# Performance work log

Measured on AMD Instinct MI355X. Metric: run time of the kernel, lower is better.

The kernel has to match this reference:

```python
import jax, jax.numpy as jnp
import numpy as np

EPS = 1e-6
B, P, C, H = 2, 2048, 256, 8
HD = C // H            # head_dims = 32
CH = C * 4             # mlp hidden = 1024


def _ln(x, g, b):
    mu = x.mean(-1, keepdims=True)
    var = ((x - mu) ** 2).mean(-1, keepdims=True)
    return (x - mu) / jnp.sqrt(var + EPS) * g + b


def _bn(x, g, b):
    # BatchNorm1d training mode on (B, Ch, L) == normalize (B,L) per channel of (B,L,Ch)
    mu = x.mean((0, 1))
    var = ((x - mu) ** 2).mean((0, 1))
    return (x - mu) / jnp.sqrt(var + EPS) * g + b


def setup_inputs() -> dict:
    key = jax.random.key(0)
    ks = jax.random.split(key, 16)
    s = 0.02
    d = {
        'x': jax.random.normal(ks[0], (B, P, C), jnp.float32),
        'ln1_g': jnp.ones((C,), jnp.float32), 'ln1_b': jnp.zeros((C,), jnp.float32),
        'ln2_g': jnp.ones((C,), jnp.float32), 'ln2_b': jnp.zeros((C,), jnp.float32),
        'Wq': jax.random.normal(ks[1], (C, C), jnp.float32) * s,
        'bq': jnp.zeros((C,), jnp.float32),
        'Wk': jax.random.normal(ks[2], (C, C), jnp.float32) * s,
        'bk': jnp.zeros((C,), jnp.float32),
        'Wv': jax.random.normal(ks[3], (C, C), jnp.float32) * s,
        'bv': jnp.zeros((C,), jnp.float32),
        'Wp': jax.random.normal(ks[4], (C, C), jnp.float32) * s,
        'bp': jnp.zeros((C,), jnp.float32),
        'W1': jax.random.normal(ks[5], (C, CH), jnp.float32) * s,
        'b1': jnp.zeros((CH,), jnp.float32),
        'bn1_g': jnp.ones((CH,), jnp.float32), 'bn1_b': jnp.zeros((CH,), jnp.float32),
        'W2': jax.random.normal(ks[6], (CH, C), jnp.float32) * s,
        'b2': jnp.zeros((C,), jnp.float32),
        'bn2_g': jnp.ones((C,), jnp.float32), 'bn2_b': jnp.zeros((C,), jnp.float32),
    }
    return d


def reference(x, ln1_g, ln1_b, ln2_g, ln2_b, Wq, bq, Wk, bk, Wv, bv, Wp, bp,
              W1, b1, bn1_g, bn1_b, W2, b2, bn2_g, bn2_b):
    lnx = _ln(x, ln1_g, ln1_b)
    # NOTE: channel-interleaved head split (view(B,P,HD,H)), faithful to source
    q = (lnx @ Wq + bq).reshape(B, P, HD, H)
    k = (lnx @ Wk + bk).reshape(B, P, HD, H)
    v = (lnx @ Wv + bv).reshape(B, P, HD, H)
    scores = jnp.einsum('bqdh,bkdh->bhqk', q, k) / np.sqrt(HD).astype(np.float32)
    w = jax.nn.softmax(scores, axis=-1)                       # (B,H,P,P)
    head = jnp.einsum('bhqk,bkdh->bhqd', w, v)                # (B,H,P,HD)
    # torch.cat(heads, -1): head0 block first -> (B,P,H,HD) flatten
    attn = head.transpose(0, 2, 1, 3).reshape(B, P, C) @ Wp + bp
    x = x + attn
    ln2x = _ln(x, ln2_g, ln2_b)
    h = jax.nn.gelu(_bn(ln2x @ W1 + b1, bn1_g, bn1_b), approximate=False)
    h = _bn(h @ W2 + b2, bn2_g, bn2_b)
    x = x + h
    fuse_weights = w[:, H - 1]          # last head's softmax weights (B,P,P)
    fuse_v = v[:, :, :, H - 1]          # last head's values (B,P,HD)
    return (x, fuse_weights, fuse_v)
```

## Files before the change

### kernel.cpp

```cpp
#include <hip/hip_runtime.h>
#include <math.h>

typedef __attribute__((ext_vector_type(8))) __bf16 bf16x8;
typedef __attribute__((ext_vector_type(4))) float f32x4;

#define NROWS 4096
#define NCe   1048576

__global__ __launch_bounds__(256) void prep_kernel(
    const float* __restrict__ Wq, const float* __restrict__ Wk,
    const float* __restrict__ Wv, const float* __restrict__ Wp,
    const float* __restrict__ W1, const float* __restrict__ W2,
    const float* __restrict__ bq, const float* __restrict__ bk,
    const float* __restrict__ bv,
    __bf16* __restrict__ wqkvT, __bf16* __restrict__ wpT,
    __bf16* __restrict__ w1T, __bf16* __restrict__ w2T,
    float* __restrict__ bqkv)
{
    int bid = blockIdx.x;
    if (bid == 768) {
        for (int i=0;i<3;i++){
            int t = i*256 + threadIdx.x;
            int h = (t>>5)&7, d = t&31;
            int c = d*8 + h;
            const float* bsrc = (t<256) ? bq : (t<512 ? bk : bv);
            bqkv[t] = bsrc[c];
        }
        return;
    }
    const float* src; __bf16* dst; int R, C, tr, tc;
    bool permute = false;
    if (bid < 256) {
        int which = bid>>6, t = bid&63;
        src = (which==0)?Wq:(which==1)?Wk:(which==2)?Wv:Wp;
        dst = (which<3) ? (wqkvT + which*65536) : wpT;
        permute = (which<3);
        R=256; C=256; tr=t>>3; tc=t&7;
    } else if (bid < 512) {
        int t = bid-256; src=W1; dst=w1T; R=256; C=1024; tr=t>>5; tc=t&31;
    } else {
        int t = bid-512; src=W2; dst=w2T; R=1024; C=256; tr=t>>3; tc=t&7;
    }
    __shared__ float tile[32][33];
    int r = threadIdx.x>>5, c = threadIdx.x&31;
    #pragma unroll
    for (int i=0;i<4;i++)
        tile[r + i*8][c] = src[(size_t)(tr*32 + r + i*8)*C + tc*32 + c];
    __syncthreads();
    #pragma unroll
    for (int i=0;i<4;i++){
        int n = tc*32 + i*8 + r;
        int nn = permute ? (((n&7)<<5) | (n>>3)) : n;
        dst[(size_t)nn*R + tr*32 + c] = (__bf16)tile[c][i*8 + r];
    }
}

__global__ __launch_bounds__(256) void ln_kernel(const float* __restrict__ x,
        const float* __restrict__ g, const float* __restrict__ b,
        __bf16* __restrict__ out)
{
    int row = blockIdx.x, t = threadIdx.x;
    float v = x[(size_t)row*256 + t];
    __shared__ float red[4];
    float s = v;
    #pragma unroll
    for (int off=32; off; off>>=1) s += __shfl_xor(s, off, 64);
    int wave = t>>6, lane = t&63;
    if (lane==0) red[wave]=s;
    __syncthreads();
    float mu = (red[0]+red[1]+red[2]+red[3]) * (1.f/256);
    float d = v - mu;
    float s2 = d*d;
    #pragma unroll
    for (int off=32; off; off>>=1) s2 += __shfl_xor(s2, off, 64);
    __syncthreads();
    if (lane==0) red[wave]=s2;
    __syncthreads();
    float var = (red[0]+red[1]+red[2]+red[3]) * (1.f/256);
    out[(size_t)row*256 + t] = (__bf16)(d * rsqrtf(var + 1e-6f) * g[t] + b[t]);
}

template<int EP>
__global__ __launch_bounds__(256) void mm_kernel(
    const __bf16* __restrict__ A, const __bf16* __restrict__ Bt,
    const float* __restrict__ bias, const float* __restrict__ resid,
    void* __restrict__ outp, float* __restrict__ out2,
    int M, int N, int K)
{
    __shared__ __bf16 Alds[128*64];
    __shared__ __bf16 Blds[128*64];
    const int tid = threadIdx.x;
    const int bm = blockIdx.y*128, bn = blockIdx.x*128;
    const int w = tid>>6, l = tid&63;
    const int wr = w>>1, wc = w&1;
    const int lg = l>>4, ll = l&15;
    f32x4 acc[4][4] = {};
    int sr[4], sc[4];
    #pragma unroll
    for (int i=0;i<4;i++){ int s = tid + i*256; sr[i]=s>>3; sc[i]=s&7; }

    for (int k0=0; k0<K; k0+=64){
        bf16x8 av[4], bv[4];
        #pragma unroll
        for (int i=0;i<4;i++){
            av[i] = *(const bf16x8*)(A  + (size_t)(bm+sr[i])*K + k0 + sc[i]*8);
            bv[i] = *(const bf16x8*)(Bt + (size_t)(bn+sr[i])*K + k0 + sc[i]*8);
        }
        __syncthreads();
        #pragma unroll
        for (int i=0;i<4;i++){
            int cc = sc[i] ^ (sr[i]&7);
            *(bf16x8*)(&Alds[sr[i]*64 + cc*8]) = av[i];
            *(bf16x8*)(&Blds[sr[i]*64 + cc*8]) = bv[i];
        }
        __syncthreads();
        #pragma unroll
        for (int kk=0; kk<2; kk++){
            bf16x8 af[4], bfr[4];
            #pragma unroll
            for (int t=0;t<4;t++){
                int ar = wr*64 + t*16 + ll;
                int ac = (kk*4 + lg) ^ (ar&7);
                af[t] = *(const bf16x8*)(&Alds[ar*64 + ac*8]);
                int br = wc*64 + t*16 + ll;
                int bc = (kk*4 + lg) ^ (br&7);
                bfr[t] = *(const bf16x8*)(&Blds[br*64 + bc*8]);
            }
            #pragma unroll
            for (int i=0;i<4;i++)
                #pragma unroll
                for (int j=0;j<4;j++)
                    acc[i][j] = __builtin_amdgcn_mfma_f32_16x16x32_bf16(af[i], bfr[j], acc[i][j], 0,0,0);
        }
    }
    #pragma unroll
    for (int i=0;i<4;i++){
        #pragma unroll
        for (int j=0;j<4;j++){
            #pragma unroll
            for (int r=0;r<4;r++){
                int m = bm + wr*64 + i*16 + lg*4 + r;
                int n = bn + wc*64 + j*16 + ll;
                float val = acc[i][j][r] + bias[n];
                if (EP == 0){
                    int kind = n>>8, h = (n>>5)&7, d = n&31;
                    int b = m>>11, p = m&2047;
                    __bf16* q = (__bf16*)outp;
                    size_t addr = (((size_t)(b*8+h))*2048 + p)*32 + d;
                    if (kind==0)      q[addr] = (__bf16)val;
                    else if (kind==1) q[NCe + addr] = (__bf16)val;
                    else {
                        q[2*NCe + addr] = (__bf16)val;
                        if (h==7) out2[((size_t)(b*2048+p))*32 + d] = val;
                    }
                } else {
                    ((__bf16*)outp)[(size_t)m*N + n] = (__bf16)val;
                }
            }
        }
    }
}

template<int EP>
__global__ __launch_bounds__(256) void mm64_kernel(
    const __bf16* __restrict__ A, const __bf16* __restrict__ Bt,
    const float* __restrict__ bias, const float* __restrict__ resid,
    void* __restrict__ outp, int M, int N, int K)
{
    __shared__ __bf16 Alds[64*64];
    __shared__ __bf16 Blds[64*64];
    const int tid = threadIdx.x;
    const int bm = blockIdx.y*64, bn = blockIdx.x*64;
    const int w = tid>>6, l = tid&63;
    const int lg = l>>4, ll = l&15;
    f32x4 acc[4] = {};
    int sr[2], sc[2];
    #pragma unroll
    for (int i=0;i<2;i++){ int s = tid + i*256; sr[i]=s>>3; sc[i]=s&7; }

    for (int k0=0; k0<K; k0+=64){
        bf16x8 av[2], bv[2];
        #pragma unroll
        for (int i=0;i<2;i++){
            av[i] = *(const bf16x8*)(A  + (size_t)(bm+sr[i])*K + k0 + sc[i]*8);
            bv[i] = *(const bf16x8*)(Bt + (size_t)(bn+sr[i])*K + k0 + sc[i]*8);
        }
        __syncthreads();
        #pragma unroll
        for (int i=0;i<2;i++){
            int cc = sc[i] ^ (sr[i]&7);
            *(bf16x8*)(&Alds[sr[i]*64 + cc*8]) = av[i];
            *(bf16x8*)(&Blds[sr[i]*64 + cc*8]) = bv[i];
        }
        __syncthreads();
        #pragma unroll
        for (int kk=0; kk<2; kk++){
            int ar = w*16 + ll;
            int ac = (kk*4 + lg) ^ (ar&7);
            bf16x8 af = *(const bf16x8*)(&Alds[ar*64 + ac*8]);
            #pragma unroll
            for (int j=0;j<4;j++){
                int br = j*16 + ll;
                int bc = (kk*4 + lg) ^ (br&7);
                bf16x8 bfr = *(const bf16x8*)(&Blds[br*64 + bc*8]);
                acc[j] = __builtin_amdgcn_mfma_f32_16x16x32_bf16(af, bfr, acc[j], 0,0,0);
            }
        }
        __syncthreads();
    }
    #pragma unroll
    for (int j=0;j<4;j++){
        #pragma unroll
        for (int r=0;r<4;r++){
            int m = bm + w*16 + lg*4 + r;
            int n = bn + j*16 + ll;
            float val = acc[j][r] + bias[n];
            if (EP == 1){
                size_t idx = (size_t)m*N + n;
                ((float*)outp)[idx] = val + resid[idx];
            } else {
                ((__bf16*)outp)[(size_t)m*N + n] = (__bf16)val;
            }
        }
    }
}

__global__ __launch_bounds__(256) void vtrans_kernel(
    const __bf16* __restrict__ vh, __bf16* __restrict__ vt)
{
    int bh = blockIdx.x>>5, d = blockIdx.x&31;
    const __bf16* src = vh + (size_t)bh*65536 + d;
    __bf16* dst = vt + (size_t)bh*65536 + (size_t)d*2048;
    int tid = threadIdx.x;
    bf16x8 v;
    #pragma unroll
    for (int j=0;j<8;j++) v[j] = src[(size_t)(tid*8+j)*32];
    *(bf16x8*)(dst + tid*8) = v;
}

__global__ __launch_bounds__(256) void attn_kernel(
    const __bf16* __restrict__ qh, const __bf16* __restrict__ kh,
    const __bf16* __restrict__ vt, __bf16* __restrict__ Oc,
    float* __restrict__ lbuf)
{
    __shared__ __bf16 Klds[64*32];
    __shared__ __bf16 Vlds[32*64];
    __shared__ __bf16 Plds[4][16*72];
    const float kScale = 0.17677669529663687f;
    int tid = threadIdx.x, w = tid>>6, l = tid&63;
    int lg = l>>4, ll = l&15;
    int bh = blockIdx.y;
    int q0 = blockIdx.x*64 + w*16;
    const __bf16* Qh = qh + (size_t)bh*65536;
    const __bf16* Kh = kh + (size_t)bh*65536;
    const __bf16* Vh = vt + (size_t)bh*65536;
    bf16x8 qf = *(const bf16x8*)(Qh + (size_t)(q0 + ll)*32 + lg*8);
    f32x4 o0 = {0,0,0,0}, o1 = {0,0,0,0};
    float lrow[4] = {0,0,0,0};
    int kr = tid>>2, kc = tid&3;
    int vr = tid>>3, vc = tid&7;
    __bf16* P = Plds[w];
    for (int kt=0; kt<2048; kt+=64){
        bf16x8 kv = *(const bf16x8*)(Kh + (size_t)(kt + kr)*32 + kc*8);
        bf16x8 vv = *(const bf16x8*)(Vh + (size_t)vr*2048 + kt + vc*8);
        __syncthreads();
        *(bf16x8*)(&Klds[kr*32 + (kc ^ ((kr>>1)&3))*8]) = kv;
        *(bf16x8*)(&Vlds[vr*64 + (vc ^ (vr&7))*8]) = vv;
        __syncthreads();
        f32x4 s[4];
        #pragma unroll
        for (int t=0;t<4;t++){
            int krow = t*16 + ll;
            bf16x8 kf = *(const bf16x8*)(&Klds[krow*32 + (lg ^ ((krow>>1)&3))*8]);
            f32x4 z = {0,0,0,0};
            s[t] = __builtin_amdgcn_mfma_f32_16x16x32_bf16(qf, kf, z, 0,0,0);
        }
        #pragma unroll
        for (int t=0;t<4;t++){
            #pragma unroll
            for (int r=0;r<4;r++){
                float p = __expf(s[t][r]*kScale);
                lrow[r] += p;
                P[(lg*4+r)*72 + t*16 + ll] = (__bf16)p;
            }
        }
        #pragma unroll
        for (int kc2=0;kc2<2;kc2++){
            bf16x8 pf = *(const bf16x8*)(&P[ll*72 + kc2*32 + lg*8]);
            int vch = kc2*4 + lg;
            int vrow0 = ll;
            bf16x8 vf0 = *(const bf16x8*)(&Vlds[vrow0*64 + (vch ^ (vrow0&7))*8]);
            o0 = __builtin_amdgcn_mfma_f32_16x16x32_bf16(pf, vf0, o0, 0,0,0);
            int vrow1 = 16 + ll;
            bf16x8 vf1 = *(const bf16x8*)(&Vlds[vrow1*64 + (vch ^ (vrow1&7))*8]);
            o1 = __builtin_amdgcn_mfma_f32_16x16x32_bf16(pf, vf1, o1, 0,0,0);
        }
    }
    #pragma unroll
    for (int r=0;r<4;r++){
        float sum = lrow[r];
        sum += __shfl_xor(sum,1,64);
        sum += __shfl_xor(sum,2,64);
        sum += __shfl_xor(sum,4,64);
        sum += __shfl_xor(sum,8,64);
        lrow[r] = sum;
    }
    int b = bh>>3, h = bh&7;
    #pragma unroll
    for (int r=0;r<4;r++){
        float inv = 1.f/lrow[r];
        int p = q0 + lg*4 + r;
        size_t base = ((size_t)(b*2048 + p))*256 + h*32;
        Oc[base + ll]      = (__bf16)(o0[r]*inv);
        Oc[base + 16 + ll] = (__bf16)(o1[r]*inv);
        if (ll==0) lbuf[(size_t)bh*2048 + p] = lrow[r];
    }
}

__global__ __launch_bounds__(256) void w7_kernel(const __bf16* __restrict__ qh,
    const __bf16* __restrict__ kh, const float* __restrict__ lbuf,
    float* __restrict__ out1)
{
    __shared__ float Qs[16][32];
    __shared__ float Li[16];
    __shared__ float Ks[256][33];
    int tid = threadIdx.x;
    int b = blockIdx.x>>7, q0 = (blockIdx.x&127)*16;
    int bh = b*8+7;
    const __bf16* Kb = kh + (size_t)bh*65536;
    const float kScale = 0.17677669529663687f;
    #pragma unroll
    for (int i=0;i<2;i++){
        int e = i*256 + tid;
        Qs[e>>5][e&31] = (float)qh[((size_t)bh*2048 + q0 + (e>>5))*32 + (e&31)];
    }
    if (tid<16) Li[tid] = 1.f/lbuf[(size_t)bh*2048 + q0 + tid];

    for (int kt=0; kt<2048; kt+=256){
        __syncthreads();
        #pragma unroll
        for (int i=0;i<4;i++){
            int e = i*256 + tid;
            int row = e>>2, d0 = (e&3)*8;
            bf16x8 kv = *(const bf16x8*)(Kb + (size_t)(kt+row)*32 + d0);
            #pragma unroll
            for (int j=0;j<8;j++) Ks[row][d0+j] = (float)kv[j];
        }
        __syncthreads();
        #pragma unroll 4
        for (int ql=0; ql<16; ql++){
            float a = 0.f;
            #pragma unroll
            for (int d=0; d<32; d++) a = fmaf(Qs[ql][d], Ks[tid][d], a);
            out1[((size_t)(b*2048 + q0 + ql))*2048 + kt + tid] =
                __expf(a*kScale)*Li[ql];
        }
    }
}

template<int NCH, int RPB>
__global__ __launch_bounds__(256) void bn_stats(const __bf16* __restrict__ h,
                                                float* __restrict__ sums)
{
    int c  = blockIdx.x*256 + threadIdx.x;
    int r0 = blockIdx.y*RPB;
    float s = 0.f, s2 = 0.f;
    #pragma unroll
    for (int i=0;i<RPB;i++){
        float v = (float)h[(size_t)(r0+i)*NCH + c];
        s += v; s2 = fmaf(v,v,s2);
    }
    atomicAdd(&sums[c], s);
    atomicAdd(&sums[NCH+c], s2);
}

template<bool GELU, bool RESID, bool OUTF32>
__global__ __launch_bounds__(256) void bn_apply(const __bf16* __restrict__ hin,
    const float* __restrict__ sums, const float* __restrict__ g,
    const float* __restrict__ bb, const float* __restrict__ resid,
    void* __restrict__ outp, int Nch)
{
    size_t i0 = ((size_t)blockIdx.x*256 + threadIdx.x)*8;
    int c0 = (int)(i0 & (size_t)(Nch-1));
    bf16x8 v = *(const bf16x8*)(hin + i0);
    float res[8];
    #pragma unroll
    for (int j=0;j<8;j++){
        int c = c0+j;
        float mu  = sums[c]*(1.f/NROWS);
        float var = sums[Nch+c]*(1.f/NROWS) - mu*mu;
        float f = ((float)v[j]-mu)*rsqrtf(var+1e-6f)*g[c]+bb[c];
        if (GELU) f = 0.5f*f*(1.f+erff(f*0.70710678118654752f));
        res[j] = f;
    }
    if (RESID){
        f32x4 r0 = *(const f32x4*)(resid+i0);
        f32x4 r1 = *(const f32x4*)(resid+i0+4);
        res[0]+=r0[0]; res[1]+=r0[1]; res[2]+=r0[2]; res[3]+=r0[3];
        res[4]+=r1[0]; res[5]+=r1[1]; res[6]+=r1[2]; res[7]+=r1[3];
    }
    if (OUTF32){
        f32x4 a = {res[0],res[1],res[2],res[3]};
        f32x4 b2 = {res[4],res[5],res[6],res[7]};
        *(f32x4*)((float*)outp + i0) = a;
        *(f32x4*)((float*)outp + i0 + 4) = b2;
    } else {
        bf16x8 ov;
        #pragma unroll
        for (int j=0;j<8;j++) ov[j] = (__bf16)res[j];
        *(bf16x8*)((__bf16*)outp + i0) = ov;
    }
}

extern "C" void kernel_launch(void* const* d_in, const int* in_sizes, int n_in,
                              void* d_out, int out_size, void* d_ws, size_t ws_size,
                              hipStream_t stream) {
    (void)in_sizes; (void)n_in; (void)out_size; (void)ws_size;
    const float* x    = (const float*)d_in[0];
    const float* ln1g = (const float*)d_in[1];
    const float* ln1b = (const float*)d_in[2];
    const float* ln2g = (const float*)d_in[3];
    const float* ln2b = (const float*)d_in[4];
    const float* Wq = (const float*)d_in[5];
    const float* bq = (const float*)d_in[6];
    const float* Wk = (const float*)d_in[7];
    const float* bk = (const float*)d_in[8];
    const float* Wv = (const float*)d_in[9];
    const float* bv = (const float*)d_in[10];
    const float* Wp = (const float*)d_in[11];
    const float* bp = (const float*)d_in[12];
    const float* W1 = (const float*)d_in[13];
    const float* b1 = (const float*)d_in[14];
    const float* bn1g = (const float*)d_in[15];
    const float* bn1b = (const float*)d_in[16];
    const float* W2 = (const float*)d_in[17];
    const float* b2 = (const float*)d_in[18];
    const float* bn2g = (const float*)d_in[19];
    const float* bn2b = (const float*)d_in[20];

    float* out0 = (float*)d_out;
    float* out1 = out0 + (size_t)NROWS*256;
    float* out2 = out1 + (size_t)2*2048*2048;

    __bf16* lnx = (__bf16*)d_ws;
    __bf16* qh  = lnx + NCe;
    __bf16* kh  = qh  + NCe;
    __bf16* vt  = kh  + NCe;
    __bf16* Oc  = vt  + NCe;
    __bf16* h1  = Oc  + NCe;
    __bf16* h1g = h1  + (size_t)NROWS*1024;
    __bf16* h2  = h1g + (size_t)NROWS*1024;
    float*  x2  = (float*)(h2 + NCe);
    float*  mbuf = x2 + NCe;
    float*  lbuf = mbuf + 32768;
    float*  bns  = lbuf + 32768;
    float*  bns2 = bns + 2048;
    float*  bqkv = bns2 + 512;
    __bf16* wqkvT = (__bf16*)(bqkv + 768);
    __bf16* wpT = wqkvT + 196608;
    __bf16* w1T = wpT + 65536;
    __bf16* w2T = w1T + 262144;
    __bf16* vh  = w2T + 262144;

    dim3 blk(256);

    hipLaunchKernelGGL(prep_kernel, dim3(769), blk, 0, stream,
        Wq,Wk,Wv,Wp,W1,W2,bq,bk,bv, wqkvT,wpT,w1T,w2T,bqkv);
    hipLaunchKernelGGL(ln_kernel, dim3(NROWS), blk, 0, stream, x, ln1g, ln1b, lnx);
    hipLaunchKernelGGL((mm_kernel<0>), dim3(6,32), blk, 0, stream,
        lnx, wqkvT, bqkv, nullptr, (void*)qh, out2, NROWS, 768, 256);
    hipLaunchKernelGGL(vtrans_kernel, dim3(512), blk, 0, stream, vh, vt);
    hipLaunchKernelGGL(attn_kernel, dim3(32,16), blk, 0, stream, qh, kh, vt, Oc, lbuf);
    hipLaunchKernelGGL(w7_kernel, dim3(256), blk, 0, stream, qh, kh, lbuf, out1);
    hipLaunchKernelGGL((mm64_kernel<1>), dim3(4,64), blk, 0, stream,
        Oc, wpT, bp, x, (void*)x2, NROWS, 256, 256);
    hipLaunchKernelGGL(ln_kernel, dim3(NROWS), blk, 0, stream, x2, ln2g, ln2b, lnx);
    hipLaunchKernelGGL((mm_kernel<2>), dim3(8,32), blk, 0, stream,
        lnx, w1T, b1, nullptr, (void*)h1, nullptr, NROWS, 1024, 256);
    hipMemsetAsync(bns, 0, 2048*sizeof(float), stream);
    hipLaunchKernelGGL((bn_stats<1024,16>), dim3(4,256), blk, 0, stream, h1, bns);
    hipLaunchKernelGGL((bn_apply<true,false,false>), dim3(2048), blk, 0, stream,
        h1, bns, bn1g, bn1b, nullptr, (void*)h1g, 1024);
    hipLaunchKernelGGL((mm64_kernel<2>), dim3(4,64), blk, 0, stream,
        h1g, w2T, b2, nullptr, (void*)h2, NROWS, 256, 1024);
    hipMemsetAsync(bns2, 0, 512*sizeof(float), stream);
    hipLaunchKernelGGL((bn_stats<256,16>), dim3(1,256), blk, 0, stream, h2, bns2);
    hipLaunchKernelGGL((bn_apply<false,true,true>), dim3(512), blk, 0, stream,
        h2, bns2, bn2g, bn2b, x2, (void*)out0, 256);
}
```

Measured before the change: 288.4 us.

## Prefetch next K tile into registers in GEMM and attention loops; merge memsets

The GEMM kernels and the attention kernel now issue the global loads for the next tile into registers right after the LDS store barrier, so those loads overlap the MFMA compute on the current tile. In mm64 the trailing barrier is removed, since the barrier before the LDS store already orders reuse. The two BN-stat memsets are merged into one issued early. The cost is higher register pressure, which could lower occupancy.

Result: faster. 279.6 us (-3.1%).

```diff
diff --git a/kernel.cpp b/kernel.cpp
--- a/kernel.cpp
+++ b/kernel.cpp
@@ -99,13 +99,13 @@
     #pragma unroll
     for (int i=0;i<4;i++){ int s = tid + i*256; sr[i]=s>>3; sc[i]=s&7; }
 
+    bf16x8 av[4], bv[4];
+    #pragma unroll
+    for (int i=0;i<4;i++){
+        av[i] = *(const bf16x8*)(A  + (size_t)(bm+sr[i])*K + sc[i]*8);
+        bv[i] = *(const bf16x8*)(Bt + (size_t)(bn+sr[i])*K + sc[i]*8);
+    }
     for (int k0=0; k0<K; k0+=64){
-        bf16x8 av[4], bv[4];
-        #pragma unroll
-        for (int i=0;i<4;i++){
-            av[i] = *(const bf16x8*)(A  + (size_t)(bm+sr[i])*K + k0 + sc[i]*8);
-            bv[i] = *(const bf16x8*)(Bt + (size_t)(bn+sr[i])*K + k0 + sc[i]*8);
-        }
         __syncthreads();
         #pragma unroll
         for (int i=0;i<4;i++){
@@ -114,6 +114,13 @@
             *(bf16x8*)(&Blds[sr[i]*64 + cc*8]) = bv[i];
         }
         __syncthreads();
+        if (k0+64 < K){
+            #pragma unroll
+            for (int i=0;i<4;i++){
+                av[i] = *(const bf16x8*)(A  + (size_t)(bm+sr[i])*K + k0+64 + sc[i]*8);
+                bv[i] = *(const bf16x8*)(Bt + (size_t)(bn+sr[i])*K + k0+64 + sc[i]*8);
+            }
+        }
         #pragma unroll
         for (int kk=0; kk<2; kk++){
             bf16x8 af[4], bfr[4];
@@ -178,13 +185,13 @@
     #pragma unroll
     for (int i=0;i<2;i++){ int s = tid + i*256; sr[i]=s>>3; sc[i]=s&7; }
 
+    bf16x8 av[2], bv[2];
+    #pragma unroll
+    for (int i=0;i<2;i++){
+        av[i] = *(const bf16x8*)(A  + (size_t)(bm+sr[i])*K + sc[i]*8);
+        bv[i] = *(const bf16x8*)(Bt + (size_t)(bn+sr[i])*K + sc[i]*8);
+    }
     for (int k0=0; k0<K; k0+=64){
-        bf16x8 av[2], bv[2];
-        #pragma unroll
-        for (int i=0;i<2;i++){
-            av[i] = *(const bf16x8*)(A  + (size_t)(bm+sr[i])*K + k0 + sc[i]*8);
-            bv[i] = *(const bf16x8*)(Bt + (size_t)(bn+sr[i])*K + k0 + sc[i]*8);
-        }
         __syncthreads();
         #pragma unroll
         for (int i=0;i<2;i++){
@@ -193,6 +200,13 @@
             *(bf16x8*)(&Blds[sr[i]*64 + cc*8]) = bv[i];
         }
         __syncthreads();
+        if (k0+64 < K){
+            #pragma unroll
+            for (int i=0;i<2;i++){
+                av[i] = *(const bf16x8*)(A  + (size_t)(bm+sr[i])*K + k0+64 + sc[i]*8);
+                bv[i] = *(const bf16x8*)(Bt + (size_t)(bn+sr[i])*K + k0+64 + sc[i]*8);
+            }
+        }
         #pragma unroll
         for (int kk=0; kk<2; kk++){
             int ar = w*16 + ll;
@@ -206,7 +220,6 @@
                 acc[j] = __builtin_amdgcn_mfma_f32_16x16x32_bf16(af, bfr, acc[j], 0,0,0);
             }
         }
-        __syncthreads();
     }
     #pragma unroll
     for (int j=0;j<4;j++){
@@ -260,13 +273,17 @@
     int kr = tid>>2, kc = tid&3;
     int vr = tid>>3, vc = tid&7;
     __bf16* P = Plds[w];
+    bf16x8 kv = *(const bf16x8*)(Kh + (size_t)kr*32 + kc*8);
+    bf16x8 vv = *(const bf16x8*)(Vh + (size_t)vr*2048 + vc*8);
     for (int kt=0; kt<2048; kt+=64){
-        bf16x8 kv = *(const bf16x8*)(Kh + (size_t)(kt + kr)*32 + kc*8);
-        bf16x8 vv = *(const bf16x8*)(Vh + (size_t)vr*2048 + kt + vc*8);
         __syncthreads();
         *(bf16x8*)(&Klds[kr*32 + (kc ^ ((kr>>1)&3))*8]) = kv;
         *(bf16x8*)(&Vlds[vr*64 + (vc ^ (vr&7))*8]) = vv;
         __syncthreads();
+        if (kt+64 < 2048){
+            kv = *(const bf16x8*)(Kh + (size_t)(kt+64 + kr)*32 + kc*8);
+            vv = *(const bf16x8*)(Vh + (size_t)vr*2048 + kt+64 + vc*8);
+        }
         f32x4 s[4];
         #pragma unroll
         for (int t=0;t<4;t++){
@@ -466,6 +483,7 @@
 
     hipLaunchKernelGGL(prep_kernel, dim3(769), blk, 0, stream,
         Wq,Wk,Wv,Wp,W1,W2,bq,bk,bv, wqkvT,wpT,w1T,w2T,bqkv);
+    hipMemsetAsync(bns, 0, 2560*sizeof(float), stream);
     hipLaunchKernelGGL(ln_kernel, dim3(NROWS), blk, 0, stream, x, ln1g, ln1b, lnx);
     hipLaunchKernelGGL((mm_kernel<0>), dim3(6,32), blk, 0, stream,
         lnx, wqkvT, bqkv, nullptr, (void*)qh, out2, NROWS, 768, 256);
@@ -477,13 +495,11 @@
     hipLaunchKernelGGL(ln_kernel, dim3(NROWS), blk, 0, stream, x2, ln2g, ln2b, lnx);
     hipLaunchKernelGGL((mm_kernel<2>), dim3(8,32), blk, 0, stream,
         lnx, w1T, b1, nullptr, (void*)h1, nullptr, NROWS, 1024, 256);
-    hipMemsetAsync(bns, 0, 2048*sizeof(float), stream);
     hipLaunchKernelGGL((bn_stats<1024,16>), dim3(4,256), blk, 0, stream, h1, bns);
     hipLaunchKernelGGL((bn_apply<true,false,false>), dim3(2048), blk, 0, stream,
         h1, bns, bn1g, bn1b, nullptr, (void*)h1g, 1024);
     hipLaunchKernelGGL((mm64_kernel<2>), dim3(4,64), blk, 0, stream,
         h1g, w2T, b2, nullptr, (void*)h2, NROWS, 256, 1024);
-    hipMemsetAsync(bns2, 0, 512*sizeof(float), stream);
     hipLaunchKernelGGL((bn_stats<256,16>), dim3(1,256), blk, 0, stream, h2, bns2);
     hipLaunchKernelGGL((bn_apply<false,true,true>), dim3(512), blk, 0, stream,
         h2, bns2, bn2g, bn2b, x2, (void*)out0, 256);
```
